# Optimization experiments

Hardware: AMD Instinct MI355X
Metric: run time of the kernel (lower is better)

Reference implementation:

```python
import jax, jax.numpy as jnp
import numpy as np

LST = 64  # sparsemax frame length over time


def sparsemax(z):
    """Sparsemax over the last axis (Martins & Astudillo 2016)."""
    d = z.shape[-1]
    z_sorted = jnp.flip(jnp.sort(z, axis=-1), axis=-1)           # descending
    z_cumsum = jnp.cumsum(z_sorted, axis=-1)
    k = jnp.arange(1, d + 1, dtype=z.dtype)
    support = (1.0 + k * z_sorted) > z_cumsum                    # bool, [..., d]
    k_z = jnp.sum(support, axis=-1, keepdims=True)               # int, >=1
    tau_sum = jnp.take_along_axis(z_cumsum, k_z - 1, axis=-1)
    tau = (tau_sum - 1.0) / k_z.astype(z.dtype)
    return jnp.maximum(z - tau, 0.0)


def setup_inputs() -> dict:
    key = jax.random.key(0)
    midis_out = jax.random.normal(key, (16, 11, 65536), dtype=jnp.float32)
    return {"midis_out": midis_out}


def reference(midis_out):
    batch, n_insts, time = midis_out.shape
    lst = LST
    len_pad = (lst - time % lst) % lst
    x = jnp.pad(midis_out, ((0, 0), (0, 0), (0, len_pad)))
    t_pad = time + len_pad
    # sparsemax over instruments: (b, t, i) -> sparsemax over i -> back to (b, i, t)
    out_inst = jnp.swapaxes(sparsemax(jnp.swapaxes(x, 1, 2)), 1, 2)
    # sparsemax over fixed time blocks of length lst
    out_time = sparsemax(x.reshape(batch, n_insts, t_pad // lst, lst))
    out_time = out_time.reshape(batch, n_insts, t_pad)
    return out_inst[:, :, :time] * out_time[:, :, :time]
```

## Files before the change

kernel.cpp:

```cpp
#include <hip/hip_runtime.h>

#define B_   16
#define NI   11
#define T_   65536
#define LST  64
#define NBLK (T_ / LST)
#define ROWS 66

__device__ __forceinline__ void ce_desc(float& a, float& b) {
    float mx = fmaxf(a, b);
    float mn = fminf(a, b);
    a = mx; b = mn;
}

__global__ __launch_bounds__(256) void fused_sparsemax_kernel(
        const float* __restrict__ in, float* __restrict__ out) {
    __shared__ float ldsz[4][NI * ROWS];
    __shared__ float ldst[4][16];

    const int lane = threadIdx.x & 63;
    const int wid  = threadIdx.x >> 6;
    const int tile = blockIdx.x * 4 + wid;
    const int b    = tile >> 10;
    const int jb   = tile & (NBLK - 1);

    const size_t base = (size_t)b * NI * T_ + (size_t)jb * LST + (size_t)lane;
    const float* px = in + base;
    float* po = out + base;

    float z[NI];
#pragma unroll
    for (int i = 0; i < NI; ++i) z[i] = px[(size_t)i * T_];

    float s[NI];
#pragma unroll
    for (int i = 0; i < NI; ++i) s[i] = z[i];
#pragma unroll
    for (int p = 0; p < NI; ++p) {
#pragma unroll
        for (int k = (p & 1); k + 1 < NI; k += 2) ce_desc(s[k], s[k + 1]);
    }
    int kz = 0;
    {
        float cum = 0.0f;
#pragma unroll
        for (int k = 1; k <= NI; ++k) {
            cum += s[k - 1];
            kz += (1.0f + (float)k * s[k - 1] > cum) ? 1 : 0;
        }
    }
    float tau_sum = 0.0f;
    {
        float cum = 0.0f;
#pragma unroll
        for (int k = 1; k <= NI; ++k) {
            cum += s[k - 1];
            if (k == kz) tau_sum = cum;
        }
    }
    const float tau_inst = (tau_sum - 1.0f) / (float)kz;

#pragma unroll
    for (int i = 0; i < NI; ++i) ldsz[wid][i * ROWS + lane] = z[i];

    const int g   = lane >> 2;
    const int q   = lane & 3;
    const int row = (g < NI) ? g : (g - NI);

    float y[16];
#pragma unroll
    for (int r = 0; r < 16; ++r) y[r] = ldsz[wid][row * ROWS + q * 16 + r];

    float s_all = 0.0f;
#pragma unroll
    for (int r = 0; r < 16; ++r) s_all += y[r];
    s_all += __shfl_xor(s_all, 1, 64);
    s_all += __shfl_xor(s_all, 2, 64);
    float tau = (s_all - 1.0f) * (1.0f / 64.0f);
    int prev = 64;

    for (int it = 0; it < 64; ++it) {
        float sp = 0.0f, cp = 0.0f;
#pragma unroll
        for (int r = 0; r < 16; ++r) {
            bool a = y[r] > tau;
            sp += a ? y[r] : 0.0f;
            cp += a ? 1.0f : 0.0f;
        }
        sp += __shfl_xor(sp, 1, 64);
        sp += __shfl_xor(sp, 2, 64);
        cp += __shfl_xor(cp, 1, 64);
        cp += __shfl_xor(cp, 2, 64);
        int cnt = (int)cp;
        bool changed = (cnt != prev);
        if (!__any(changed)) break;
        prev = cnt;
        tau  = (sp - 1.0f) / cp;
    }

    if (g < NI && q == 0) ldst[wid][g] = tau;

    float tt[NI];
#pragma unroll
    for (int i = 0; i < NI; ++i) tt[i] = ldst[wid][i];

#pragma unroll
    for (int i = 0; i < NI; ++i) {
        float oi = fmaxf(z[i] - tt[i], 0.0f) * fmaxf(z[i] - tau_inst, 0.0f);
        po[(size_t)i * T_] = oi;
    }
}

extern "C" void kernel_launch(void* const* d_in, const int* in_sizes, int n_in,
                              void* d_out, int out_size, void* d_ws, size_t ws_size,
                              hipStream_t stream) {
    const float* in = (const float*)d_in[0];
    float* out = (float*)d_out;
    hipLaunchKernelGGL(fused_sparsemax_kernel, dim3(4096), dim3(256), 0, stream,
                       in, out);
}
```

Baseline: 28.48 us.

## Replace instrument sort with fixed-point sparsemax and vectorize output stores

Replaces the 11-element odd-even sort for the instrument sparsemax with a Michelot-style fixed-point iteration that starts from max-1. The time-block iteration also starts from max-1 instead of the mean, and the divides become hardware reciprocal approximations. The output is written from the transposed row layout with float4 stores instead of strided scalar stores, with the instrument tau passed through shared memory. The intent is to cut ALU work and store instructions. The cost is a data-dependent loop count and an approximate reciprocal that can shift tau by a few ulps.

```diff
diff --git a/kernel.cpp b/kernel.cpp
--- a/kernel.cpp
+++ b/kernel.cpp
@@ -5,18 +5,14 @@
 #define T_   65536
 #define LST  64
 #define NBLK (T_ / LST)
-#define ROWS 66
+#define ROWP 68
 
-__device__ __forceinline__ void ce_desc(float& a, float& b) {
-    float mx = fmaxf(a, b);
-    float mn = fminf(a, b);
-    a = mx; b = mn;
-}
+__device__ __forceinline__ float frcp(float x) { return __builtin_amdgcn_rcpf(x); }
 
 __global__ __launch_bounds__(256) void fused_sparsemax_kernel(
         const float* __restrict__ in, float* __restrict__ out) {
-    __shared__ float ldsz[4][NI * ROWS];
-    __shared__ float ldst[4][16];
+    __shared__ float ldsz[4][NI * ROWP];
+    __shared__ float ldsti[4][64];
 
     const int lane = threadIdx.x & 63;
     const int wid  = threadIdx.x >> 6;
@@ -24,44 +20,34 @@
     const int b    = tile >> 10;
     const int jb   = tile & (NBLK - 1);
 
-    const size_t base = (size_t)b * NI * T_ + (size_t)jb * LST + (size_t)lane;
-    const float* px = in + base;
-    float* po = out + base;
+    const float* px = in + (size_t)b * NI * T_ + (size_t)jb * LST + (size_t)lane;
 
     float z[NI];
 #pragma unroll
     for (int i = 0; i < NI; ++i) z[i] = px[(size_t)i * T_];
 
-    float s[NI];
 #pragma unroll
-    for (int i = 0; i < NI; ++i) s[i] = z[i];
+    for (int i = 0; i < NI; ++i) ldsz[wid][i * ROWP + lane] = z[i];
+
+    float mx = z[0];
 #pragma unroll
-    for (int p = 0; p < NI; ++p) {
+    for (int i = 1; i < NI; ++i) mx = fmaxf(mx, z[i]);
+    float tau_i = mx - 1.0f;
+    float prevc = 0.0f;
+    for (int it = 0; it < NI + 2; ++it) {
+        float sp = 0.0f, cp = 0.0f;
 #pragma unroll
-        for (int k = (p & 1); k + 1 < NI; k += 2) ce_desc(s[k], s[k + 1]);
+        for (int i = 0; i < NI; ++i) {
+            bool a = z[i] > tau_i;
+            sp += a ? z[i] : 0.0f;
+            cp += a ? 1.0f : 0.0f;
+        }
+        bool changed = (cp != prevc);
+        if (!__any(changed)) break;
+        prevc = cp;
+        tau_i = (sp - 1.0f) * frcp(cp);
     }
-    int kz = 0;
-    {
-        float cum = 0.0f;
-#pragma unroll
-        for (int k = 1; k <= NI; ++k) {
-            cum += s[k - 1];
-            kz += (1.0f + (float)k * s[k - 1] > cum) ? 1 : 0;
-        }
-    }
-    float tau_sum = 0.0f;
-    {
-        float cum = 0.0f;
-#pragma unroll
-        for (int k = 1; k <= NI; ++k) {
-            cum += s[k - 1];
-            if (k == kz) tau_sum = cum;
-        }
-    }
-    const float tau_inst = (tau_sum - 1.0f) / (float)kz;
-
-#pragma unroll
-    for (int i = 0; i < NI; ++i) ldsz[wid][i * ROWS + lane] = z[i];
+    ldsti[wid][lane] = tau_i;
 
     const int g   = lane >> 2;
     const int q   = lane & 3;
@@ -69,17 +55,16 @@
 
     float y[16];
 #pragma unroll
-    for (int r = 0; r < 16; ++r) y[r] = ldsz[wid][row * ROWS + q * 16 + r];
+    for (int r = 0; r < 16; ++r) y[r] = ldsz[wid][row * ROWP + q * 16 + r];
 
-    float s_all = 0.0f;
+    float m = y[0];
 #pragma unroll
-    for (int r = 0; r < 16; ++r) s_all += y[r];
-    s_all += __shfl_xor(s_all, 1, 64);
-    s_all += __shfl_xor(s_all, 2, 64);
-    float tau = (s_all - 1.0f) * (1.0f / 64.0f);
-    int prev = 64;
-
-    for (int it = 0; it < 64; ++it) {
+    for (int r = 1; r < 16; ++r) m = fmaxf(m, y[r]);
+    m = fmaxf(m, __shfl_xor(m, 1, 64));
+    m = fmaxf(m, __shfl_xor(m, 2, 64));
+    float tau = m - 1.0f;
+    float prev = 0.0f;
+    for (int it = 0; it < LST + 2; ++it) {
         float sp = 0.0f, cp = 0.0f;
 #pragma unroll
         for (int r = 0; r < 16; ++r) {
@@ -91,23 +76,29 @@
         sp += __shfl_xor(sp, 2, 64);
         cp += __shfl_xor(cp, 1, 64);
         cp += __shfl_xor(cp, 2, 64);
-        int cnt = (int)cp;
-        bool changed = (cnt != prev);
+        bool changed = (cp != prev);
         if (!__any(changed)) break;
-        prev = cnt;
-        tau  = (sp - 1.0f) / cp;
+        prev = cp;
+        tau = (sp - 1.0f) * frcp(cp);
     }
 
-    if (g < NI && q == 0) ldst[wid][g] = tau;
+    if (g < NI) {
+        float ti[16];
+#pragma unroll
+        for (int r = 0; r < 16; ++r) ti[r] = ldsti[wid][q * 16 + r];
 
-    float tt[NI];
+        float* po = out + (size_t)b * NI * T_ + (size_t)g * T_
+                        + (size_t)jb * LST + (size_t)q * 16;
+        float4* po4 = reinterpret_cast<float4*>(po);
 #pragma unroll
-    for (int i = 0; i < NI; ++i) tt[i] = ldst[wid][i];
-
-#pragma unroll
-    for (int i = 0; i < NI; ++i) {
-        float oi = fmaxf(z[i] - tt[i], 0.0f) * fmaxf(z[i] - tau_inst, 0.0f);
-        po[(size_t)i * T_] = oi;
+        for (int v = 0; v < 4; ++v) {
+            float4 o;
+            o.x = fmaxf(y[4*v+0] - tau, 0.0f) * fmaxf(y[4*v+0] - ti[4*v+0], 0.0f);
+            o.y = fmaxf(y[4*v+1] - tau, 0.0f) * fmaxf(y[4*v+1] - ti[4*v+1], 0.0f);
+            o.z = fmaxf(y[4*v+2] - tau, 0.0f) * fmaxf(y[4*v+2] - ti[4*v+2], 0.0f);
+            o.w = fmaxf(y[4*v+3] - tau, 0.0f) * fmaxf(y[4*v+3] - ti[4*v+3], 0.0f);
+            po4[v] = o;
+        }
     }
 }
 
```

New measurement: 27.57 us. 3.2% less time.
